# Optimization experiments

Measured on AMD Instinct MI355X. Metric: run time of the kernel, lower is better.

The kernel has to match this reference:

```python
import jax, jax.numpy as jnp
import numpy as np

NUM_TOKENS = 4096
HIDDEN = 2048
INTER = 1408
NUM_EXPERTS = 8
TOP_K = 2


def setup_inputs() -> dict:
    key = jax.random.key(0)
    k1, k2, k3, k4, k5 = jax.random.split(key, 5)
    hidden_states = jax.random.normal(k1, (NUM_TOKENS, HIDDEN), dtype=jnp.float32)
    # w1: (E, 2*I, H) gate+up fused; w2: (E, H, I)
    w1 = jax.random.normal(k2, (NUM_EXPERTS, 2 * INTER, HIDDEN), dtype=jnp.float32) * (1.0 / np.sqrt(HIDDEN))
    w2 = jax.random.normal(k3, (NUM_EXPERTS, HIDDEN, INTER), dtype=jnp.float32) * (1.0 / np.sqrt(INTER))
    raw = jax.random.uniform(k4, (NUM_TOKENS, TOP_K), dtype=jnp.float32)
    topk_weights = raw / jnp.sum(raw, axis=-1, keepdims=True)  # router softmax-normalized weights
    topk_ids = jax.random.randint(k5, (NUM_TOKENS, TOP_K), 0, NUM_EXPERTS, dtype=jnp.int32)
    return {"hidden_states": hidden_states, "w1": w1, "w2": w2,
            "topk_weights": topk_weights, "topk_ids": topk_ids}


def reference(hidden_states, w1, w2, topk_weights, topk_ids):
    """Math-equivalent of fused_experts (dispatch -> grouped gate_up GEMM ->
    SwiGLU -> grouped down GEMM -> weighted scatter-combine).

    Expressed densely per expert (E is small and fixed), which yields the
    identical output to the sorted/grouped-GEMM formulation.
    """
    E = w1.shape[0]
    inter = w1.shape[1] // 2
    dtype = hidden_states.dtype
    # gate_up projection for every expert: [E, N, 2I]
    gate_up = jnp.einsum('nh,eih->eni', hidden_states, w1)
    gate, up = gate_up[..., :inter], gate_up[..., inter:]
    act = jax.nn.silu(gate) * up  # npu_swiglu: silu(first half) * second half
    # down projection: [E, N, H]
    expert_out = jnp.einsum('eni,ehi->enh', act, w2)
    # combine weight per (token, expert): sum of topk_weights where routed
    one_hot = jax.nn.one_hot(topk_ids, E, dtype=dtype)          # [N, K, E]
    combine = jnp.sum(topk_weights[:, :, None] * one_hot, axis=1)  # [N, E]
    return jnp.einsum('ne,enh->nh', combine, expert_out)
```

## Files before the change

### kernel.cpp

```cpp
#include <hip/hip_runtime.h>
#include <hip/hip_bf16.h>

#define NTOK 4096
#define HID 2048
#define INTER 1408
#define NEXP 8
#define NPAIR 8192
#define NKT1 32
#define NKT2 22
#define SZ2 16384

typedef short bf16x8 __attribute__((ext_vector_type(8)));
typedef float f32x4 __attribute__((ext_vector_type(4)));

__device__ __forceinline__ unsigned short f2bf(float f) {
  unsigned u = __builtin_bit_cast(unsigned, f);
  u += 0x7fffu + ((u >> 16) & 1u);
  return (unsigned short)(u >> 16);
}
__device__ __forceinline__ float bf2f(unsigned short v) {
  return __builtin_bit_cast(float, (unsigned)v << 16);
}

__device__ __forceinline__ void gload16(const void* g, void* l) {
  __builtin_amdgcn_global_load_lds(
      (const __attribute__((address_space(1))) void*)g,
      (__attribute__((address_space(3))) void*)l, 16, 0, 0);
}

__device__ __forceinline__ int xcd_swz(int lin, int nwg) {
  int xcd = lin & 7, base = lin >> 3;
  int q = nwg >> 3, r = nwg & 7;
  return (xcd < r ? xcd * (q + 1) : r * (q + 1) + (xcd - r) * q) + base;
}

#define BAR __builtin_amdgcn_s_barrier()
#define LGKM0 asm volatile("s_waitcnt lgkmcnt(0)" ::: "memory")
#define VM6 asm volatile("s_waitcnt vmcnt(6)" ::: "memory")
#define VM0 asm volatile("s_waitcnt vmcnt(0)" ::: "memory")
#define PRIO1 __builtin_amdgcn_s_setprio(1)
#define PRIO0 __builtin_amdgcn_s_setprio(0)

__global__ void k_cvt_all(const float* __restrict__ hs, const float* __restrict__ w1,
                          const float* __restrict__ w2, unsigned short* __restrict__ dst) {
  const int N0 = NTOK * HID / 4;
  const int N1 = N0 + NEXP * 2 * INTER * HID / 4;
  const int N2 = N1 + NEXP * HID * INTER / 4;
  int i = blockIdx.x * blockDim.x + threadIdx.x;
  int stride = gridDim.x * blockDim.x;
  for (; i < N2; i += stride) {
    const float* s; int o;
    if (i < N0) { s = hs; o = i; }
    else if (i < N1) { s = w1; o = i - N0; }
    else { s = w2; o = i - N1; }
    float4 v = reinterpret_cast<const float4*>(s)[o];
    ushort4 u;
    u.x = f2bf(v.x); u.y = f2bf(v.y); u.z = f2bf(v.z); u.w = f2bf(v.w);
    reinterpret_cast<ushort4*>(dst)[i] = u;
  }
}

__global__ void k_route(const int* __restrict__ ids, int* __restrict__ ctrl,
                        unsigned short* __restrict__ row_token,
                        unsigned short* __restrict__ inv_row) {
  __shared__ int cnt[NEXP], cur[NEXP];
  int t = threadIdx.x;
  if (t < NEXP) cnt[t] = 0;
  __syncthreads();
  for (int p = t; p < NPAIR; p += 512) atomicAdd(&cnt[ids[p]], 1);
  __syncthreads();
  if (t == 0) {
    int acc = 0, T1 = 0, T2 = 0;
    for (int e = 0; e < NEXP; ++e) {
      cur[e] = acc;
      ctrl[e] = cnt[e];
      ctrl[8 + e] = acc;
      int n1 = (cnt[e] + 255) >> 8;
      for (int m = 0; m < n1; ++m) { ctrl[32 + T1] = e; ctrl[71 + T1] = m; ++T1; }
      int n2 = (cnt[e] + 127) >> 7;
      for (int m = 0; m < n2; ++m) { ctrl[110 + T2] = e; ctrl[181 + T2] = m; ++T2; }
      acc += cnt[e];
    }
    ctrl[16] = T1;
    ctrl[17] = T2;
  }
  __syncthreads();
  for (int p = t; p < NPAIR; p += 512) {
    int e = ids[p];
    int pos = atomicAdd(&cur[e], 1);
    row_token[pos] = (unsigned short)(p >> 1);
    inv_row[p] = (unsigned short)pos;
  }
}


#define G1_STAGE_A(BB, u, ktile) \
  gload16(asrc[(u)*2+0] + (ktile)*64, lds + (BB) + ((u)*2+0)*4096 + wvb); \
  gload16(asrc[(u)*2+1] + (ktile)*64, lds + (BB) + ((u)*2+1)*4096 + wvb);
#define G1_STAGE_B(BB, u, ktile) \
  gload16(bsrc[(u)*2+0] + (ktile)*64, lds + (BB) + 16384 + ((u)*2+0)*4096 + wvb); \
  gload16(bsrc[(u)*2+1] + (ktile)*64, lds + (BB) + 16384 + ((u)*2+1)*4096 + wvb);

#define G1_READ_A(dst, BB, mh) \
  _Pragma("unroll") for (int m_ = 0; m_ < 4; ++m_) { \
    dst[m_][0] = *(const bf16x8*)(lds + (BB) + aoff + (mh)*8192 + m_*1024 + csw0); \
    dst[m_][1] = *(const bf16x8*)(lds + (BB) + aoff + (mh)*8192 + m_*1024 + csw1); \
  }
#define G1_READ_B(dst, BB, nh) \
  _Pragma("unroll") for (int n_ = 0; n_ < 2; ++n_) { \
    dst[n_][0] = *(const bf16x8*)(lds + (BB) + boff + (nh)*8192 + n_*1024 + csw0); \
    dst[n_][1] = *(const bf16x8*)(lds + (BB) + boff + (nh)*8192 + n_*1024 + csw1); \
  }

#define G1_MMA_Q(afr, bfr, mh, nh) \
  _Pragma("unroll") for (int m_ = 0; m_ < 4; ++m_) \
  _Pragma("unroll") for (int n_ = 0; n_ < 2; ++n_) { \
    acc[(mh)*4+m_][(nh)*2+n_] = __builtin_amdgcn_mfma_f32_16x16x32_bf16(afr[m_][0], bfr[n_][0], acc[(mh)*4+m_][(nh)*2+n_], 0, 0, 0); \
    acc[(mh)*4+m_][(nh)*2+n_] = __builtin_amdgcn_mfma_f32_16x16x32_bf16(afr[m_][1], bfr[n_][1], acc[(mh)*4+m_][(nh)*2+n_], 0, 0, 0); \
  }

#define G1_EIGHT(kt) \
  G1_READ_A(afM0, 0, 0) G1_READ_B(bfN0, 0, 0) G1_STAGE_B(32768, 1, (kt)+1); \
  BAR; LGKM0; PRIO1; G1_MMA_Q(afM0, bfN0, 0, 0) PRIO0; BAR; \
  G1_READ_B(bfN1, 0, 1) G1_STAGE_B(0, 0, (kt)+2); \
  BAR; LGKM0; PRIO1; G1_MMA_Q(afM0, bfN1, 0, 1) PRIO0; BAR; \
  G1_READ_A(afM1, 0, 1) G1_STAGE_A(0, 0, (kt)+2); \
  BAR; LGKM0; PRIO1; G1_MMA_Q(afM1, bfN1, 1, 1) PRIO0; BAR; \
  G1_STAGE_A(0, 1, (kt)+2); \
  BAR; LGKM0; PRIO1; G1_MMA_Q(afM1, bfN0, 1, 0) PRIO0; VM6; BAR; \
  G1_READ_A(afM0, 32768, 0) G1_READ_B(bfN0, 32768, 0) G1_STAGE_B(0, 1, (kt)+2); \
  BAR; LGKM0; PRIO1; G1_MMA_Q(afM0, bfN0, 0, 0) PRIO0; BAR; \
  G1_READ_B(bfN1, 32768, 1) G1_STAGE_B(32768, 0, (kt)+3); \
  BAR; LGKM0; PRIO1; G1_MMA_Q(afM0, bfN1, 0, 1) PRIO0; BAR; \
  G1_READ_A(afM1, 32768, 1) G1_STAGE_A(32768, 0, (kt)+3); \
  BAR; LGKM0; PRIO1; G1_MMA_Q(afM1, bfN1, 1, 1) PRIO0; BAR; \
  G1_STAGE_A(32768, 1, (kt)+3); \
  BAR; LGKM0; PRIO1; G1_MMA_Q(afM1, bfN0, 1, 0) PRIO0; VM6; BAR;

#define G1_EPI(kt) \
  G1_READ_A(afM0, 0, 0) G1_READ_B(bfN0, 0, 0) G1_STAGE_B(32768, 1, (kt)+1); \
  BAR; LGKM0; PRIO1; G1_MMA_Q(afM0, bfN0, 0, 0) PRIO0; BAR; \
  G1_READ_B(bfN1, 0, 1) \
  BAR; LGKM0; PRIO1; G1_MMA_Q(afM0, bfN1, 0, 1) PRIO0; BAR; \
  G1_READ_A(afM1, 0, 1) \
  BAR; LGKM0; PRIO1; G1_MMA_Q(afM1, bfN1, 1, 1) PRIO0; BAR; \
  BAR; LGKM0; PRIO1; G1_MMA_Q(afM1, bfN0, 1, 0) PRIO0; VM0; BAR; \
  G1_READ_A(afM0, 32768, 0) G1_READ_B(bfN0, 32768, 0) \
  BAR; LGKM0; PRIO1; G1_MMA_Q(afM0, bfN0, 0, 0) PRIO0; BAR; \
  G1_READ_B(bfN1, 32768, 1) \
  BAR; LGKM0; PRIO1; G1_MMA_Q(afM0, bfN1, 0, 1) PRIO0; BAR; \
  G1_READ_A(afM1, 32768, 1) \
  BAR; LGKM0; PRIO1; G1_MMA_Q(afM1, bfN1, 1, 1) PRIO0; BAR; \
  LGKM0; PRIO1; G1_MMA_Q(afM1, bfN0, 1, 0) PRIO0;

__global__ __launch_bounds__(512, 2) void k_gemm1(
    const unsigned short* __restrict__ hs,
    const unsigned short* __restrict__ w1,
    const int* __restrict__ ctrl,
    const unsigned short* __restrict__ row_token,
    unsigned short* __restrict__ act) {
  const int T1 = ctrl[16];
  const int nwg = T1 * 11;
  const int lin = blockIdx.x;
  if (lin >= nwg) return;
  const int wg = xcd_swz(lin, nwg);
  const int ti = wg / 11;
  const int nt = wg - ti * 11;
  const int e = ctrl[32 + ti], mt = ctrl[71 + ti];
  const int rows = ctrl[e], off_e = ctrl[8 + e];
  const int n0g = nt * 128;
  const unsigned short* w1e = w1 + (size_t)e * (2 * INTER * HID);

  __shared__ unsigned short smem[65536];
  unsigned short* lds = smem;

  const int t = threadIdx.x;
  const int lane = t & 63, wv = t >> 6;
  const int wm = wv >> 2, wn = wv & 3;
  const int lm = lane & 15, hi4 = lane >> 4;
  const int wvb = (t & 448) * 8;
  const int aoff = (wm * 64 + lm) * 64;
  const int boff = 16384 + (wn * 32 + lm) * 64;
  const int csw0 = (hi4 ^ (lm & 7)) * 8;
  const int csw1 = ((4 + hi4) ^ (lm & 7)) * 8;

  const unsigned short* asrc[4];
#pragma unroll
  for (int i = 0; i < 4; ++i) {
    int p = i * 64 + (t >> 3);
    int r = ((p >> 6) & 1) * 128 + (p >> 7) * 64 + (p & 63);
    int grow = mt * 256 + r;
    if (grow > rows - 1) grow = rows - 1;
    int token = row_token[off_e + grow];
    asrc[i] = hs + (size_t)token * HID + ((t & 7) ^ (p & 7)) * 8;
  }
  const unsigned short* bsrc[4];
#pragma unroll
  for (int i = 0; i < 4; ++i) {
    int p = i * 64 + (t >> 3);
    int nh = p >> 7, wns = (p & 127) >> 5, idx = p & 31;
    int c = n0g + wns * 32 + idx + nh * INTER;
    bsrc[i] = w1e + (size_t)c * HID + ((t & 7) ^ (p & 7)) * 8;
  }

  f32x4 acc[8][4];
#pragma unroll
  for (int i = 0; i < 8; ++i)
#pragma unroll
    for (int j = 0; j < 4; ++j) acc[i][j] = (f32x4){0.f, 0.f, 0.f, 0.f};
  bf16x8 afM0[4][2], afM1[4][2], bfN0[2][2], bfN1[2][2];

  G1_STAGE_B(0, 0, 0) G1_STAGE_A(0, 0, 0) G1_STAGE_A(0, 1, 0) G1_STAGE_B(0, 1, 0)
  G1_STAGE_B(32768, 0, 1) G1_STAGE_A(32768, 0, 1) G1_STAGE_A(32768, 1, 1)
  VM6; BAR;

  for (int kt = 0; kt + 3 < NKT1; kt += 2) { G1_EIGHT(kt) }
  G1_EPI(NKT1 - 2)

#pragma unroll
  for (int mh = 0; mh < 2; ++mh)
#pragma unroll
    for (int m = 0; m < 4; ++m)
#pragma unroll
      for (int n = 0; n < 2; ++n) {
        int col = n0g + wn * 32 + n * 16 + lm;
#pragma unroll
        for (int j = 0; j < 4; ++j) {
          int grow = mt * 256 + wm * 128 + mh * 64 + m * 16 + hi4 * 4 + j;
          if (grow < rows) {
            float g = acc[mh * 4 + m][n][j];
            float u = acc[mh * 4 + m][2 + n][j];
            float a = g / (1.0f + __expf(-g)) * u;
            act[(size_t)(off_e + grow) * INTER + col] = f2bf(a);
          }
        }
      }
}

#define G2_RD_A(BB) { \
  _Pragma("unroll") for (int m_ = 0; m_ < 4; ++m_) { \
    af[m_][0] = *(const bf16x8*)(smem + (BB) + aoff + m_*1024 + csw0); \
    af[m_][1] = *(const bf16x8*)(smem + (BB) + aoff + m_*1024 + csw1); } }
#define G2_RD_B(BB) { \
  _Pragma("unroll") for (int n_ = 0; n_ < 2; ++n_) { \
    bfr[n_][0] = *(const bf16x8*)(smem + (BB) + boff + n_*1024 + csw0); \
    bfr[n_][1] = *(const bf16x8*)(smem + (BB) + boff + n_*1024 + csw1); } }

__global__ __launch_bounds__(512, 4) void k_gemm2(
    const unsigned short* __restrict__ act,
    const unsigned short* __restrict__ w2,
    const int* __restrict__ ctrl,
    unsigned short* __restrict__ eo) {
  const int T2 = ctrl[17];
  const int nwg = T2 * 16;
  const int lin = blockIdx.x;
  if (lin >= nwg) return;
  const int wg = xcd_swz(lin, nwg);
  const int ti = wg >> 4;
  const int nt = wg & 15;
  const int e = ctrl[110 + ti], mt = ctrl[181 + ti];
  const int rows = ctrl[e], off_e = ctrl[8 + e];
  const int n0 = nt * 128;
  const unsigned short* w2e = w2 + (size_t)e * (HID * INTER);

  __shared__ unsigned short smem[SZ2 * 2];

  const int t = threadIdx.x;
  const int lane = t & 63, wv = t >> 6;
  const int wm = wv >> 2, wn = wv & 3;
  const int lm = lane & 15, hi4 = lane >> 4;
  const int aoff = (wm * 64 + lm) * 64;
  const int boff = 8192 + (wn * 32 + lm) * 64;
  const int csw0 = (hi4 ^ (lm & 7)) * 8;
  const int csw1 = ((4 + hi4) ^ (lm & 7)) * 8;
  const int ldst = t * 8;

  const unsigned short* asrc[2];
#pragma unroll
  for (int i = 0; i < 2; ++i) {
    int p = i * 512 + t;
    int row = p >> 3, c = p & 7;
    int grow = mt * 128 + row;
    if (grow > rows - 1) grow = rows - 1;
    asrc[i] = act + (size_t)(off_e + grow) * INTER + (c ^ (row & 7)) * 8;
  }
  const unsigned short* bsrc[2];
#pragma unroll
  for (int i = 0; i < 2; ++i) {
    int p = i * 512 + t;
    int cb = p >> 3, c = p & 7;
    bsrc[i] = w2e + (size_t)(n0 + cb) * INTER + (c ^ (cb & 7)) * 8;
  }

#define G2_STAGE(BB, kt) { \
  gload16(asrc[0] + (size_t)(kt)*64, smem + (BB) + ldst); \
  gload16(asrc[1] + (size_t)(kt)*64, smem + (BB) + 4096 + ldst); \
  gload16(bsrc[0] + (size_t)(kt)*64, smem + (BB) + 8192 + ldst); \
  gload16(bsrc[1] + (size_t)(kt)*64, smem + (BB) + 12288 + ldst); }

  f32x4 acc[4][2];
#pragma unroll
  for (int m = 0; m < 4; ++m)
#pragma unroll
    for (int n = 0; n < 2; ++n) acc[m][n] = (f32x4){0.f, 0.f, 0.f, 0.f};
  bf16x8 af[4][2], bfr[2][2];

  unsigned cur = 0, oth = SZ2;
  G2_STAGE(cur, 0)
  VM0; BAR;

  for (int kt = 0; kt < NKT2; ++kt) {
    G2_RD_A(cur)
    G2_RD_B(cur)
    if (kt + 1 < NKT2) G2_STAGE(oth, kt + 1)
    BAR; LGKM0; PRIO1;
#pragma unroll
    for (int kk = 0; kk < 2; ++kk)
#pragma unroll
      for (int m = 0; m < 4; ++m)
#pragma unroll
        for (int n = 0; n < 2; ++n)
          acc[m][n] = __builtin_amdgcn_mfma_f32_16x16x32_bf16(af[m][kk], bfr[n][kk], acc[m][n], 0, 0, 0);
    PRIO0; VM0; BAR;
    unsigned tmp = cur; cur = oth; oth = tmp;
  }

#pragma unroll
  for (int m = 0; m < 4; ++m)
#pragma unroll
    for (int n = 0; n < 2; ++n) {
      int col = n0 + wn * 32 + n * 16 + lm;
#pragma unroll
      for (int j = 0; j < 4; ++j) {
        int grow = mt * 128 + wm * 64 + m * 16 + hi4 * 4 + j;
        if (grow < rows)
          eo[(size_t)(off_e + grow) * HID + col] = f2bf(acc[m][n][j]);
      }
    }
#undef G2_STAGE
}

__global__ void k_combine(const unsigned short* __restrict__ eo,
                          const float* __restrict__ tw,
                          const unsigned short* __restrict__ inv_row,
                          float* __restrict__ out) {
  int idx = blockIdx.x * blockDim.x + threadIdx.x;
  int tok = idx >> 8;
  int c8 = (idx & 255) * 8;
  int r0 = inv_row[tok * 2], r1 = inv_row[tok * 2 + 1];
  float w0 = tw[tok * 2], w1 = tw[tok * 2 + 1];
  bf16x8 v0 = *(const bf16x8*)(eo + (size_t)r0 * HID + c8);
  bf16x8 v1 = *(const bf16x8*)(eo + (size_t)r1 * HID + c8);
  float4 o0, o1;
  o0.x = w0 * bf2f((unsigned short)v0[0]) + w1 * bf2f((unsigned short)v1[0]);
  o0.y = w0 * bf2f((unsigned short)v0[1]) + w1 * bf2f((unsigned short)v1[1]);
  o0.z = w0 * bf2f((unsigned short)v0[2]) + w1 * bf2f((unsigned short)v1[2]);
  o0.w = w0 * bf2f((unsigned short)v0[3]) + w1 * bf2f((unsigned short)v1[3]);
  o1.x = w0 * bf2f((unsigned short)v0[4]) + w1 * bf2f((unsigned short)v1[4]);
  o1.y = w0 * bf2f((unsigned short)v0[5]) + w1 * bf2f((unsigned short)v1[5]);
  o1.z = w0 * bf2f((unsigned short)v0[6]) + w1 * bf2f((unsigned short)v1[6]);
  o1.w = w0 * bf2f((unsigned short)v0[7]) + w1 * bf2f((unsigned short)v1[7]);
  float4* op = reinterpret_cast<float4*>(out) + (size_t)tok * 512 + (idx & 255) * 2;
  op[0] = o0;
  op[1] = o1;
}

extern "C" void kernel_launch(void* const* d_in, const int* in_sizes, int n_in,
                              void* d_out, int out_size, void* d_ws, size_t ws_size,
                              hipStream_t stream) {
  const float* hs_f = (const float*)d_in[0];
  const float* w1_f = (const float*)d_in[1];
  const float* w2_f = (const float*)d_in[2];
  const float* tw   = (const float*)d_in[3];
  const int*   tids = (const int*)d_in[4];
  float* out = (float*)d_out;

  char* ws = (char*)d_ws;
  unsigned short* hs_b = (unsigned short*)(ws);
  unsigned short* w1_b = (unsigned short*)(ws + 16777216);
  unsigned short* w2_b = (unsigned short*)(ws + 109051904);
  unsigned short* act  = (unsigned short*)(ws + 155189248);
  unsigned short* eo   = (unsigned short*)(ws + 16777216);
  int* ctrl = (int*)(ws + 178257920);
  unsigned short* row_token = (unsigned short*)(ws + 178258944);
  unsigned short* inv_row   = (unsigned short*)(ws + 178275328);

  k_route<<<1, 512, 0, stream>>>(tids, ctrl, row_token, inv_row);
  k_cvt_all<<<4096, 256, 0, stream>>>(hs_f, w1_f, w2_f, hs_b);

  k_gemm1<<<39 * 11, 512, 0, stream>>>(hs_b, w1_b, ctrl, row_token, act);
  k_gemm2<<<71 * 16, 512, 0, stream>>>(act, w2_b, ctrl, eo);
  k_combine<<<NTOK * HID / 8 / 256, 256, 0, stream>>>(eo, tw, inv_row, out);
}
```

Measured before the change: 285.6 us.

## Load fp32 weights directly in GEMMs, converting to bf16 on LDS read

Removes the separate pass that converts w1 and w2 to bf16. The GEMM kernels now stream the fp32 weights straight into LDS and convert them to bf16 while building MFMA fragments; only the hidden states are still pre-converted. This drops one full read-and-write of the weights in exchange for larger fp32 LDS tiles, half-depth K tiles (twice as many iterations), extra conversion ALU work in the inner loop, and reworked swizzles and pipelines. Grid sizes and the ctrl table offsets are also enlarged.

Measured after the change: 410.7 us. 43.8% more time.

```diff
diff --git a/kernel.cpp b/kernel.cpp
--- a/kernel.cpp
+++ b/kernel.cpp
@@ -6,12 +6,14 @@
 #define INTER 1408
 #define NEXP 8
 #define NPAIR 8192
-#define NKT1 32
-#define NKT2 22
-#define SZ2 16384
+#define NK1 64
+#define NK2 44
+#define G1BUF 49152
+#define G2BUF 24576
 
 typedef short bf16x8 __attribute__((ext_vector_type(8)));
 typedef float f32x4 __attribute__((ext_vector_type(4)));
+typedef unsigned u32x4 __attribute__((ext_vector_type(4)));
 
 __device__ __forceinline__ unsigned short f2bf(float f) {
   unsigned u = __builtin_bit_cast(unsigned, f);
@@ -21,6 +23,13 @@
 __device__ __forceinline__ float bf2f(unsigned short v) {
   return __builtin_bit_cast(float, (unsigned)v << 16);
 }
+__device__ __forceinline__ unsigned pk2(float lo, float hi) {
+  return (unsigned)f2bf(lo) | ((unsigned)f2bf(hi) << 16);
+}
+__device__ __forceinline__ bf16x8 cvt8(float4 a, float4 b) {
+  u32x4 u = { pk2(a.x, a.y), pk2(a.z, a.w), pk2(b.x, b.y), pk2(b.z, b.w) };
+  return __builtin_bit_cast(bf16x8, u);
+}
 
 __device__ __forceinline__ void gload16(const void* g, void* l) {
   __builtin_amdgcn_global_load_lds(
@@ -36,28 +45,16 @@
 
 #define BAR __builtin_amdgcn_s_barrier()
 #define LGKM0 asm volatile("s_waitcnt lgkmcnt(0)" ::: "memory")
-#define VM6 asm volatile("s_waitcnt vmcnt(6)" ::: "memory")
-#define VM0 asm volatile("s_waitcnt vmcnt(0)" ::: "memory")
+#define VMW(N) asm volatile("s_waitcnt vmcnt(" #N ")" ::: "memory")
 #define PRIO1 __builtin_amdgcn_s_setprio(1)
 #define PRIO0 __builtin_amdgcn_s_setprio(0)
 
-__global__ void k_cvt_all(const float* __restrict__ hs, const float* __restrict__ w1,
-                          const float* __restrict__ w2, unsigned short* __restrict__ dst) {
-  const int N0 = NTOK * HID / 4;
-  const int N1 = N0 + NEXP * 2 * INTER * HID / 4;
-  const int N2 = N1 + NEXP * HID * INTER / 4;
+__global__ void k_cvt_hs(const float* __restrict__ s, unsigned short* __restrict__ d) {
   int i = blockIdx.x * blockDim.x + threadIdx.x;
-  int stride = gridDim.x * blockDim.x;
-  for (; i < N2; i += stride) {
-    const float* s; int o;
-    if (i < N0) { s = hs; o = i; }
-    else if (i < N1) { s = w1; o = i - N0; }
-    else { s = w2; o = i - N1; }
-    float4 v = reinterpret_cast<const float4*>(s)[o];
-    ushort4 u;
-    u.x = f2bf(v.x); u.y = f2bf(v.y); u.z = f2bf(v.z); u.w = f2bf(v.w);
-    reinterpret_cast<ushort4*>(dst)[i] = u;
-  }
+  float4 v = reinterpret_cast<const float4*>(s)[i];
+  ushort4 u;
+  u.x = f2bf(v.x); u.y = f2bf(v.y); u.z = f2bf(v.z); u.w = f2bf(v.w);
+  reinterpret_cast<ushort4*>(d)[i] = u;
 }
 
 __global__ void k_route(const int* __restrict__ ids, int* __restrict__ ctrl,
@@ -76,9 +73,9 @@
       ctrl[e] = cnt[e];
       ctrl[8 + e] = acc;
       int n1 = (cnt[e] + 255) >> 8;
-      for (int m = 0; m < n1; ++m) { ctrl[32 + T1] = e; ctrl[71 + T1] = m; ++T1; }
+      for (int m = 0; m < n1; ++m) { ctrl[32 + T1] = e; ctrl[73 + T1] = m; ++T1; }
       int n2 = (cnt[e] + 127) >> 7;
-      for (int m = 0; m < n2; ++m) { ctrl[110 + T2] = e; ctrl[181 + T2] = m; ++T2; }
+      for (int m = 0; m < n2; ++m) { ctrl[114 + T2] = e; ctrl[187 + T2] = m; ++T2; }
       acc += cnt[e];
     }
     ctrl[16] = T1;
@@ -94,68 +91,71 @@
 }
 
 
-#define G1_STAGE_A(BB, u, ktile) \
-  gload16(asrc[(u)*2+0] + (ktile)*64, lds + (BB) + ((u)*2+0)*4096 + wvb); \
-  gload16(asrc[(u)*2+1] + (ktile)*64, lds + (BB) + ((u)*2+1)*4096 + wvb);
-#define G1_STAGE_B(BB, u, ktile) \
-  gload16(bsrc[(u)*2+0] + (ktile)*64, lds + (BB) + 16384 + ((u)*2+0)*4096 + wvb); \
-  gload16(bsrc[(u)*2+1] + (ktile)*64, lds + (BB) + 16384 + ((u)*2+1)*4096 + wvb);
-
-#define G1_READ_A(dst, BB, mh) \
-  _Pragma("unroll") for (int m_ = 0; m_ < 4; ++m_) { \
-    dst[m_][0] = *(const bf16x8*)(lds + (BB) + aoff + (mh)*8192 + m_*1024 + csw0); \
-    dst[m_][1] = *(const bf16x8*)(lds + (BB) + aoff + (mh)*8192 + m_*1024 + csw1); \
-  }
-#define G1_READ_B(dst, BB, nh) \
+#define G1_RDA(BB, mh) { \
+  _Pragma("unroll") for (int m_ = 0; m_ < 4; ++m_) \
+    af[m_] = *(const bf16x8*)(smem + (BB) + arow + (mh)*8192 + m_*1024 + aswz); }
+
+#define G1_RDB(dst, BB, nh) { \
   _Pragma("unroll") for (int n_ = 0; n_ < 2; ++n_) { \
-    dst[n_][0] = *(const bf16x8*)(lds + (BB) + boff + (nh)*8192 + n_*1024 + csw0); \
-    dst[n_][1] = *(const bf16x8*)(lds + (BB) + boff + (nh)*8192 + n_*1024 + csw1); \
-  }
-
-#define G1_MMA_Q(afr, bfr, mh, nh) \
+    float4 x0_ = *(const float4*)(smem + (BB) + 16384 + brow + (nh)*16384 + n_*2048 + bswz0); \
+    float4 x1_ = *(const float4*)(smem + (BB) + 16384 + brow + (nh)*16384 + n_*2048 + bswz1); \
+    dst[n_] = cvt8(x0_, x1_); } }
+
+#define G1_MMA(mh, nh, bfr) \
   _Pragma("unroll") for (int m_ = 0; m_ < 4; ++m_) \
-  _Pragma("unroll") for (int n_ = 0; n_ < 2; ++n_) { \
-    acc[(mh)*4+m_][(nh)*2+n_] = __builtin_amdgcn_mfma_f32_16x16x32_bf16(afr[m_][0], bfr[n_][0], acc[(mh)*4+m_][(nh)*2+n_], 0, 0, 0); \
-    acc[(mh)*4+m_][(nh)*2+n_] = __builtin_amdgcn_mfma_f32_16x16x32_bf16(afr[m_][1], bfr[n_][1], acc[(mh)*4+m_][(nh)*2+n_], 0, 0, 0); \
-  }
-
-#define G1_EIGHT(kt) \
-  G1_READ_A(afM0, 0, 0) G1_READ_B(bfN0, 0, 0) G1_STAGE_B(32768, 1, (kt)+1); \
-  BAR; LGKM0; PRIO1; G1_MMA_Q(afM0, bfN0, 0, 0) PRIO0; BAR; \
-  G1_READ_B(bfN1, 0, 1) G1_STAGE_B(0, 0, (kt)+2); \
-  BAR; LGKM0; PRIO1; G1_MMA_Q(afM0, bfN1, 0, 1) PRIO0; BAR; \
-  G1_READ_A(afM1, 0, 1) G1_STAGE_A(0, 0, (kt)+2); \
-  BAR; LGKM0; PRIO1; G1_MMA_Q(afM1, bfN1, 1, 1) PRIO0; BAR; \
-  G1_STAGE_A(0, 1, (kt)+2); \
-  BAR; LGKM0; PRIO1; G1_MMA_Q(afM1, bfN0, 1, 0) PRIO0; VM6; BAR; \
-  G1_READ_A(afM0, 32768, 0) G1_READ_B(bfN0, 32768, 0) G1_STAGE_B(0, 1, (kt)+2); \
-  BAR; LGKM0; PRIO1; G1_MMA_Q(afM0, bfN0, 0, 0) PRIO0; BAR; \
-  G1_READ_B(bfN1, 32768, 1) G1_STAGE_B(32768, 0, (kt)+3); \
-  BAR; LGKM0; PRIO1; G1_MMA_Q(afM0, bfN1, 0, 1) PRIO0; BAR; \
-  G1_READ_A(afM1, 32768, 1) G1_STAGE_A(32768, 0, (kt)+3); \
-  BAR; LGKM0; PRIO1; G1_MMA_Q(afM1, bfN1, 1, 1) PRIO0; BAR; \
-  G1_STAGE_A(32768, 1, (kt)+3); \
-  BAR; LGKM0; PRIO1; G1_MMA_Q(afM1, bfN0, 1, 0) PRIO0; VM6; BAR;
-
-#define G1_EPI(kt) \
-  G1_READ_A(afM0, 0, 0) G1_READ_B(bfN0, 0, 0) G1_STAGE_B(32768, 1, (kt)+1); \
-  BAR; LGKM0; PRIO1; G1_MMA_Q(afM0, bfN0, 0, 0) PRIO0; BAR; \
-  G1_READ_B(bfN1, 0, 1) \
-  BAR; LGKM0; PRIO1; G1_MMA_Q(afM0, bfN1, 0, 1) PRIO0; BAR; \
-  G1_READ_A(afM1, 0, 1) \
-  BAR; LGKM0; PRIO1; G1_MMA_Q(afM1, bfN1, 1, 1) PRIO0; BAR; \
-  BAR; LGKM0; PRIO1; G1_MMA_Q(afM1, bfN0, 1, 0) PRIO0; VM0; BAR; \
-  G1_READ_A(afM0, 32768, 0) G1_READ_B(bfN0, 32768, 0) \
-  BAR; LGKM0; PRIO1; G1_MMA_Q(afM0, bfN0, 0, 0) PRIO0; BAR; \
-  G1_READ_B(bfN1, 32768, 1) \
-  BAR; LGKM0; PRIO1; G1_MMA_Q(afM0, bfN1, 0, 1) PRIO0; BAR; \
-  G1_READ_A(afM1, 32768, 1) \
-  BAR; LGKM0; PRIO1; G1_MMA_Q(afM1, bfN1, 1, 1) PRIO0; BAR; \
-  LGKM0; PRIO1; G1_MMA_Q(afM1, bfN0, 1, 0) PRIO0;
+  _Pragma("unroll") for (int n_ = 0; n_ < 2; ++n_) \
+    acc[(mh)*4+m_][(nh)*2+n_] = __builtin_amdgcn_mfma_f32_16x16x32_bf16(af[m_], bfr[n_], acc[(mh)*4+m_][(nh)*2+n_], 0, 0, 0);
+
+#define G1_STA(BB, kt) { \
+  gload16(aptr0 + (size_t)(kt)*32, smem + (BB) + wv16); \
+  gload16(aptr1 + (size_t)(kt)*32, smem + (BB) + 8192 + wv16); }
+#define G1_STBG(BB, kt) { \
+  gload16(bptr0 + (size_t)(kt)*32, smem + (BB) + 16384 + wv16); \
+  gload16(bptr1 + (size_t)(kt)*32, smem + (BB) + 24576 + wv16); }
+#define G1_STBU(BB, kt) { \
+  gload16(bptr2 + (size_t)(kt)*32, smem + (BB) + 32768 + wv16); \
+  gload16(bptr3 + (size_t)(kt)*32, smem + (BB) + 40960 + wv16); }
+
+#define G1_TILE_FULL(CUR, OTH, kt) \
+  G1_RDA(CUR, 0) G1_RDB(bg, CUR, 0) G1_STA(OTH, (kt)+1) \
+  LGKM0; BAR; \
+  PRIO1; G1_MMA(0, 0, bg) PRIO0; BAR; \
+  G1_RDB(bu, CUR, 1) G1_STBG(CUR, (kt)+2) \
+  LGKM0; BAR; \
+  PRIO1; G1_MMA(0, 1, bu) PRIO0; BAR; \
+  G1_RDA(CUR, 1) G1_STBU(CUR, (kt)+2) \
+  LGKM0; BAR; \
+  PRIO1; G1_MMA(1, 1, bu) PRIO0; BAR; \
+  VMW(4); BAR; \
+  PRIO1; G1_MMA(1, 0, bg) PRIO0;
+
+#define G1_TILE_N2(CUR, OTH, kt) \
+  G1_RDA(CUR, 0) G1_RDB(bg, CUR, 0) G1_STA(OTH, (kt)+1) \
+  LGKM0; BAR; \
+  PRIO1; G1_MMA(0, 0, bg) PRIO0; BAR; \
+  G1_RDB(bu, CUR, 1) \
+  LGKM0; BAR; \
+  PRIO1; G1_MMA(0, 1, bu) PRIO0; BAR; \
+  G1_RDA(CUR, 1) \
+  LGKM0; BAR; \
+  PRIO1; G1_MMA(1, 1, bu) PRIO0; BAR; \
+  VMW(0); BAR; \
+  PRIO1; G1_MMA(1, 0, bg) PRIO0;
+
+#define G1_TILE_LAST(CUR) \
+  G1_RDA(CUR, 0) G1_RDB(bg, CUR, 0) \
+  LGKM0; BAR; \
+  PRIO1; G1_MMA(0, 0, bg) PRIO0; BAR; \
+  G1_RDB(bu, CUR, 1) \
+  LGKM0; BAR; \
+  PRIO1; G1_MMA(0, 1, bu) PRIO0; BAR; \
+  G1_RDA(CUR, 1) LGKM0; \
+  PRIO1; G1_MMA(1, 1, bu) PRIO0; \
+  PRIO1; G1_MMA(1, 0, bg) PRIO0;
 
 __global__ __launch_bounds__(512, 2) void k_gemm1(
     const unsigned short* __restrict__ hs,
-    const unsigned short* __restrict__ w1,
+    const float* __restrict__ w1f,
     const int* __restrict__ ctrl,
     const unsigned short* __restrict__ row_token,
     unsigned short* __restrict__ act) {
@@ -166,41 +166,41 @@
   const int wg = xcd_swz(lin, nwg);
   const int ti = wg / 11;
   const int nt = wg - ti * 11;
-  const int e = ctrl[32 + ti], mt = ctrl[71 + ti];
+  const int e = ctrl[32 + ti], mt = ctrl[73 + ti];
   const int rows = ctrl[e], off_e = ctrl[8 + e];
   const int n0g = nt * 128;
-  const unsigned short* w1e = w1 + (size_t)e * (2 * INTER * HID);
-
-  __shared__ unsigned short smem[65536];
-  unsigned short* lds = smem;
+  const float* w1e = w1f + (size_t)e * (2 * INTER * HID);
+
+  __shared__ __align__(16) char smem[2 * G1BUF];
 
   const int t = threadIdx.x;
   const int lane = t & 63, wv = t >> 6;
   const int wm = wv >> 2, wn = wv & 3;
   const int lm = lane & 15, hi4 = lane >> 4;
-  const int wvb = (t & 448) * 8;
-  const int aoff = (wm * 64 + lm) * 64;
-  const int boff = 16384 + (wn * 32 + lm) * 64;
-  const int csw0 = (hi4 ^ (lm & 7)) * 8;
-  const int csw1 = ((4 + hi4) ^ (lm & 7)) * 8;
-
-  const unsigned short* asrc[4];
-#pragma unroll
-  for (int i = 0; i < 4; ++i) {
-    int p = i * 64 + (t >> 3);
-    int r = ((p >> 6) & 1) * 128 + (p >> 7) * 64 + (p & 63);
-    int grow = mt * 256 + r;
-    if (grow > rows - 1) grow = rows - 1;
-    int token = row_token[off_e + grow];
-    asrc[i] = hs + (size_t)token * HID + ((t & 7) ^ (p & 7)) * 8;
-  }
-  const unsigned short* bsrc[4];
-#pragma unroll
-  for (int i = 0; i < 4; ++i) {
-    int p = i * 64 + (t >> 3);
-    int nh = p >> 7, wns = (p & 127) >> 5, idx = p & 31;
-    int c = n0g + wns * 32 + idx + nh * INTER;
-    bsrc[i] = w1e + (size_t)c * HID + ((t & 7) ^ (p & 7)) * 8;
+  const int wv16 = (t & 448) * 16;
+  const int arow = wm * 4096 + lm * 64;
+  const int aswz = (hi4 ^ ((lm >> 1) & 3)) * 16;
+  const int brow = wn * 4096 + lm * 128;
+  const int bswz0 = ((hi4 * 2) ^ (lm & 7)) * 16;
+  const int bswz1 = ((hi4 * 2 + 1) ^ (lm & 7)) * 16;
+
+  const unsigned short *aptr0, *aptr1;
+  {
+    int sw = ((t & 3) ^ ((t >> 3) & 3)) * 8;
+    int r0 = t >> 2, r1 = 128 + (t >> 2);
+    int g0 = mt * 256 + r0; if (g0 > rows - 1) g0 = rows - 1;
+    int g1 = mt * 256 + r1; if (g1 > rows - 1) g1 = rows - 1;
+    aptr0 = hs + (size_t)row_token[off_e + g0] * HID + sw;
+    aptr1 = hs + (size_t)row_token[off_e + g1] * HID + sw;
+  }
+  const float *bptr0, *bptr1, *bptr2, *bptr3;
+  {
+    int cl = t >> 3;
+    int bsw = ((t & 7) ^ ((t >> 3) & 7)) * 4;
+    bptr0 = w1e + (size_t)(n0g + cl) * HID + bsw;
+    bptr1 = w1e + (size_t)(n0g + 64 + cl) * HID + bsw;
+    bptr2 = w1e + (size_t)(INTER + n0g + cl) * HID + bsw;
+    bptr3 = w1e + (size_t)(INTER + n0g + 64 + cl) * HID + bsw;
   }
 
   f32x4 acc[8][4];
@@ -208,14 +208,18 @@
   for (int i = 0; i < 8; ++i)
 #pragma unroll
     for (int j = 0; j < 4; ++j) acc[i][j] = (f32x4){0.f, 0.f, 0.f, 0.f};
-  bf16x8 afM0[4][2], afM1[4][2], bfN0[2][2], bfN1[2][2];
-
-  G1_STAGE_B(0, 0, 0) G1_STAGE_A(0, 0, 0) G1_STAGE_A(0, 1, 0) G1_STAGE_B(0, 1, 0)
-  G1_STAGE_B(32768, 0, 1) G1_STAGE_A(32768, 0, 1) G1_STAGE_A(32768, 1, 1)
-  VM6; BAR;
-
-  for (int kt = 0; kt + 3 < NKT1; kt += 2) { G1_EIGHT(kt) }
-  G1_EPI(NKT1 - 2)
+  bf16x8 af[4], bg[2], bu[2];
+
+  G1_STBG(0, 0) G1_STBU(0, 0) G1_STA(0, 0)
+  G1_STBG(G1BUF, 1) G1_STBU(G1BUF, 1)
+  VMW(4); BAR;
+
+  for (int kt = 0; kt < NK1 - 2; kt += 2) {
+    G1_TILE_FULL(0, G1BUF, kt)
+    G1_TILE_FULL(G1BUF, 0, kt + 1)
+  }
+  G1_TILE_N2(0, G1BUF, NK1 - 2)
+  G1_TILE_LAST(G1BUF)
 
 #pragma unroll
   for (int mh = 0; mh < 2; ++mh)
@@ -226,7 +230,7 @@
         int col = n0g + wn * 32 + n * 16 + lm;
 #pragma unroll
         for (int j = 0; j < 4; ++j) {
-          int grow = mt * 256 + wm * 128 + mh * 64 + m * 16 + hi4 * 4 + j;
+          int grow = mt * 256 + wm * 64 + mh * 128 + m * 16 + hi4 * 4 + j;
           if (grow < rows) {
             float g = acc[mh * 4 + m][n][j];
             float u = acc[mh * 4 + m][2 + n][j];
@@ -237,18 +241,47 @@
       }
 }
 
-#define G2_RD_A(BB) { \
-  _Pragma("unroll") for (int m_ = 0; m_ < 4; ++m_) { \
-    af[m_][0] = *(const bf16x8*)(smem + (BB) + aoff + m_*1024 + csw0); \
-    af[m_][1] = *(const bf16x8*)(smem + (BB) + aoff + m_*1024 + csw1); } }
-#define G2_RD_B(BB) { \
+#define G2_RDA(lo, hi) { \
+  _Pragma("unroll") for (int m_ = (lo); m_ < (hi); ++m_) \
+    af[m_] = *(const bf16x8*)(smem + CURB + arow + m_*1024 + aswz); }
+#define G2_RDB() { \
   _Pragma("unroll") for (int n_ = 0; n_ < 2; ++n_) { \
-    bfr[n_][0] = *(const bf16x8*)(smem + (BB) + boff + n_*1024 + csw0); \
-    bfr[n_][1] = *(const bf16x8*)(smem + (BB) + boff + n_*1024 + csw1); } }
+    float4 x0_ = *(const float4*)(smem + CURB + 8192 + brow + n_*2048 + bswz0); \
+    float4 x1_ = *(const float4*)(smem + CURB + 8192 + brow + n_*2048 + bswz1); \
+    bn[n_] = cvt8(x0_, x1_); } }
+#define G2_MMA(lo, hi) \
+  _Pragma("unroll") for (int m_ = (lo); m_ < (hi); ++m_) \
+  _Pragma("unroll") for (int n_ = 0; n_ < 2; ++n_) \
+    acc[m_][n_] = __builtin_amdgcn_mfma_f32_16x16x32_bf16(af[m_], bn[n_], acc[m_][n_], 0, 0, 0);
+#define G2_STA(BB, kt) \
+  gload16(aptr + (size_t)(kt)*32, smem + (BB) + wv16);
+#define G2_STB(BB, kt) { \
+  gload16(bptr0 + (size_t)(kt)*32, smem + (BB) + 8192 + wv16); \
+  gload16(bptr1 + (size_t)(kt)*32, smem + (BB) + 16384 + wv16); }
+
+#define G2_IT_FULL(CURB_, OTH, kt) { enum { CURB = CURB_ }; \
+  G2_RDA(0, 2) G2_RDB() G2_STA(OTH, (kt)+1) \
+  LGKM0; BAR; \
+  G2_STB(CURB_, (kt)+2) G2_RDA(2, 4) \
+  PRIO1; G2_MMA(0, 2) G2_MMA(2, 4) PRIO0; \
+  VMW(2); BAR; }
+
+#define G2_IT_N2(CURB_, OTH, kt) { enum { CURB = CURB_ }; \
+  G2_RDA(0, 2) G2_RDB() G2_STA(OTH, (kt)+1) \
+  LGKM0; BAR; \
+  G2_RDA(2, 4) \
+  PRIO1; G2_MMA(0, 2) G2_MMA(2, 4) PRIO0; \
+  VMW(0); BAR; }
+
+#define G2_IT_LAST(CURB_) { enum { CURB = CURB_ }; \
+  G2_RDA(0, 2) G2_RDB() \
+  LGKM0; BAR; \
+  G2_RDA(2, 4) \
+  PRIO1; G2_MMA(0, 2) G2_MMA(2, 4) PRIO0; }
 
 __global__ __launch_bounds__(512, 4) void k_gemm2(
     const unsigned short* __restrict__ act,
-    const unsigned short* __restrict__ w2,
+    const float* __restrict__ w2f,
     const int* __restrict__ ctrl,
     unsigned short* __restrict__ eo) {
   const int T2 = ctrl[17];
@@ -258,72 +291,55 @@
   const int wg = xcd_swz(lin, nwg);
   const int ti = wg >> 4;
   const int nt = wg & 15;
-  const int e = ctrl[110 + ti], mt = ctrl[181 + ti];
+  const int e = ctrl[114 + ti], mt = ctrl[187 + ti];
   const int rows = ctrl[e], off_e = ctrl[8 + e];
   const int n0 = nt * 128;
-  const unsigned short* w2e = w2 + (size_t)e * (HID * INTER);
-
-  __shared__ unsigned short smem[SZ2 * 2];
+  const float* w2e = w2f + (size_t)e * (HID * INTER);
+
+  __shared__ __align__(16) char smem[2 * G2BUF];
 
   const int t = threadIdx.x;
   const int lane = t & 63, wv = t >> 6;
   const int wm = wv >> 2, wn = wv & 3;
   const int lm = lane & 15, hi4 = lane >> 4;
-  const int aoff = (wm * 64 + lm) * 64;
-  const int boff = 8192 + (wn * 32 + lm) * 64;
-  const int csw0 = (hi4 ^ (lm & 7)) * 8;
-  const int csw1 = ((4 + hi4) ^ (lm & 7)) * 8;
-  const int ldst = t * 8;
-
-  const unsigned short* asrc[2];
-#pragma unroll
-  for (int i = 0; i < 2; ++i) {
-    int p = i * 512 + t;
-    int row = p >> 3, c = p & 7;
-    int grow = mt * 128 + row;
-    if (grow > rows - 1) grow = rows - 1;
-    asrc[i] = act + (size_t)(off_e + grow) * INTER + (c ^ (row & 7)) * 8;
-  }
-  const unsigned short* bsrc[2];
-#pragma unroll
-  for (int i = 0; i < 2; ++i) {
-    int p = i * 512 + t;
-    int cb = p >> 3, c = p & 7;
-    bsrc[i] = w2e + (size_t)(n0 + cb) * INTER + (c ^ (cb & 7)) * 8;
-  }
-
-#define G2_STAGE(BB, kt) { \
-  gload16(asrc[0] + (size_t)(kt)*64, smem + (BB) + ldst); \
-  gload16(asrc[1] + (size_t)(kt)*64, smem + (BB) + 4096 + ldst); \
-  gload16(bsrc[0] + (size_t)(kt)*64, smem + (BB) + 8192 + ldst); \
-  gload16(bsrc[1] + (size_t)(kt)*64, smem + (BB) + 12288 + ldst); }
+  const int wv16 = (t & 448) * 16;
+  const int arow = wm * 4096 + lm * 64;
+  const int aswz = (hi4 ^ ((lm >> 1) & 3)) * 16;
+  const int brow = wn * 4096 + lm * 128;
+  const int bswz0 = ((hi4 * 2) ^ (lm & 7)) * 16;
+  const int bswz1 = ((hi4 * 2 + 1) ^ (lm & 7)) * 16;
+
+  const unsigned short* aptr;
+  {
+    int sw = ((t & 3) ^ ((t >> 3) & 3)) * 8;
+    int r = t >> 2;
+    int g0 = mt * 128 + r; if (g0 > rows - 1) g0 = rows - 1;
+    aptr = act + (size_t)(off_e + g0) * INTER + sw;
+  }
+  const float *bptr0, *bptr1;
+  {
+    int bsw = ((t & 7) ^ ((t >> 3) & 7)) * 4;
+    bptr0 = w2e + (size_t)(n0 + (t >> 3)) * INTER + bsw;
+    bptr1 = w2e + (size_t)(n0 + 64 + (t >> 3)) * INTER + bsw;
+  }
 
   f32x4 acc[4][2];
 #pragma unroll
   for (int m = 0; m < 4; ++m)
 #pragma unroll
     for (int n = 0; n < 2; ++n) acc[m][n] = (f32x4){0.f, 0.f, 0.f, 0.f};
-  bf16x8 af[4][2], bfr[2][2];
-
-  unsigned cur = 0, oth = SZ2;
-  G2_STAGE(cur, 0)
-  VM0; BAR;
-
-  for (int kt = 0; kt < NKT2; ++kt) {
-    G2_RD_A(cur)
-    G2_RD_B(cur)
-    if (kt + 1 < NKT2) G2_STAGE(oth, kt + 1)
-    BAR; LGKM0; PRIO1;
-#pragma unroll
-    for (int kk = 0; kk < 2; ++kk)
-#pragma unroll
-      for (int m = 0; m < 4; ++m)
-#pragma unroll
-        for (int n = 0; n < 2; ++n)
-          acc[m][n] = __builtin_amdgcn_mfma_f32_16x16x32_bf16(af[m][kk], bfr[n][kk], acc[m][n], 0, 0, 0);
-    PRIO0; VM0; BAR;
-    unsigned tmp = cur; cur = oth; oth = tmp;
-  }
+  bf16x8 af[4], bn[2];
+
+  G2_STB(0, 0) G2_STA(0, 0)
+  G2_STB(G2BUF, 1)
+  VMW(2); BAR;
+
+  for (int kt = 0; kt < NK2 - 2; kt += 2) {
+    G2_IT_FULL(0, G2BUF, kt)
+    G2_IT_FULL(G2BUF, 0, kt + 1)
+  }
+  G2_IT_N2(0, G2BUF, NK2 - 2)
+  G2_IT_LAST(G2BUF)
 
 #pragma unroll
   for (int m = 0; m < 4; ++m)
@@ -337,7 +353,6 @@
           eo[(size_t)(off_e + grow) * HID + col] = f2bf(acc[m][n][j]);
       }
     }
-#undef G2_STAGE
 }
 
 __global__ void k_combine(const unsigned short* __restrict__ eo,
@@ -377,18 +392,16 @@
 
   char* ws = (char*)d_ws;
   unsigned short* hs_b = (unsigned short*)(ws);
-  unsigned short* w1_b = (unsigned short*)(ws + 16777216);
-  unsigned short* w2_b = (unsigned short*)(ws + 109051904);
-  unsigned short* act  = (unsigned short*)(ws + 155189248);
-  unsigned short* eo   = (unsigned short*)(ws + 16777216);
-  int* ctrl = (int*)(ws + 178257920);
-  unsigned short* row_token = (unsigned short*)(ws + 178258944);
-  unsigned short* inv_row   = (unsigned short*)(ws + 178275328);
+  unsigned short* act  = (unsigned short*)(ws + 16777216);
+  unsigned short* eo   = (unsigned short*)(ws + 39845888);
+  int* ctrl = (int*)(ws + 73400320);
+  unsigned short* row_token = (unsigned short*)(ws + 73402368);
+  unsigned short* inv_row   = (unsigned short*)(ws + 73418752);
 
   k_route<<<1, 512, 0, stream>>>(tids, ctrl, row_token, inv_row);
-  k_cvt_all<<<4096, 256, 0, stream>>>(hs_f, w1_f, w2_f, hs_b);
-
-  k_gemm1<<<39 * 11, 512, 0, stream>>>(hs_b, w1_b, ctrl, row_token, act);
-  k_gemm2<<<71 * 16, 512, 0, stream>>>(act, w2_b, ctrl, eo);
+  k_cvt_hs<<<NTOK * HID / 4 / 256, 256, 0, stream>>>(hs_f, hs_b);
+
+  k_gemm1<<<41 * 11, 512, 0, stream>>>(hs_b, w1_f, ctrl, row_token, act);
+  k_gemm2<<<73 * 16, 512, 0, stream>>>(act, w2_f, ctrl, eo);
   k_combine<<<NTOK * HID / 8 / 256, 256, 0, stream>>>(eo, tw, inv_row, out);
 }
```

## Fuse routing into conversion, overlap w2 conversion with gemm1, retile gemm2

Applied to the files above, without the earlier changes.

Routing now runs in block 0 of a single prep kernel that also converts hidden states and w1 to bf16, which removes one launch. Converting w2 to bf16 moves into the spare blocks of the gemm1 launch (grid raised to 1024), so it can overlap with the first GEMM. gemm2 is retiled to 128x256 output tiles with a K-step of 32 and a three-stage global-to-LDS pipeline, aiming for more reuse per A load and better latency hiding. The risks are that the conversion blocks compete with gemm1 for bandwidth and compute units, and that the larger gemm2 accumulator set raises register pressure under launch_bounds(512,4).

Measured after the change: 257.8 us. -9.7%, faster.

```diff
diff --git a/kernel.cpp b/kernel.cpp
--- a/kernel.cpp
+++ b/kernel.cpp
@@ -7,8 +7,8 @@
 #define NEXP 8
 #define NPAIR 8192
 #define NKT1 32
-#define NKT2 22
-#define SZ2 16384
+#define NK2 44
+#define G2SZ 24576
 
 typedef short bf16x8 __attribute__((ext_vector_type(8)));
 typedef float f32x4 __attribute__((ext_vector_type(4)));
@@ -35,61 +35,60 @@
 }
 
 #define BAR __builtin_amdgcn_s_barrier()
+#define SCHED0 __builtin_amdgcn_sched_barrier(0)
 #define LGKM0 asm volatile("s_waitcnt lgkmcnt(0)" ::: "memory")
 #define VM6 asm volatile("s_waitcnt vmcnt(6)" ::: "memory")
+#define VM3 asm volatile("s_waitcnt vmcnt(3)" ::: "memory")
 #define VM0 asm volatile("s_waitcnt vmcnt(0)" ::: "memory")
 #define PRIO1 __builtin_amdgcn_s_setprio(1)
 #define PRIO0 __builtin_amdgcn_s_setprio(0)
 
-__global__ void k_cvt_all(const float* __restrict__ hs, const float* __restrict__ w1,
-                          const float* __restrict__ w2, unsigned short* __restrict__ dst) {
+__global__ void k_prep(const float* __restrict__ hs, const float* __restrict__ w1,
+                       unsigned short* __restrict__ dst,
+                       const int* __restrict__ ids, int* __restrict__ ctrl,
+                       unsigned short* __restrict__ row_token,
+                       unsigned short* __restrict__ inv_row) {
+  if (blockIdx.x == 0) {
+    __shared__ int cnt[NEXP], cur[NEXP];
+    int t = threadIdx.x;
+    if (t < NEXP) cnt[t] = 0;
+    __syncthreads();
+    for (int p = t; p < NPAIR; p += 512) atomicAdd(&cnt[ids[p]], 1);
+    __syncthreads();
+    if (t == 0) {
+      int acc = 0, T1 = 0, T2 = 0;
+      for (int e = 0; e < NEXP; ++e) {
+        cur[e] = acc;
+        ctrl[e] = cnt[e];
+        ctrl[8 + e] = acc;
+        int n1 = (cnt[e] + 255) >> 8;
+        for (int m = 0; m < n1; ++m) { ctrl[32 + T1] = e; ctrl[72 + T1] = m; ++T1; }
+        int n2 = (cnt[e] + 127) >> 7;
+        for (int m = 0; m < n2; ++m) { ctrl[112 + T2] = e; ctrl[184 + T2] = m; ++T2; }
+        acc += cnt[e];
+      }
+      ctrl[16] = T1;
+      ctrl[17] = T2;
+    }
+    __syncthreads();
+    for (int p = t; p < NPAIR; p += 512) {
+      int e = ids[p];
+      int pos = atomicAdd(&cur[e], 1);
+      row_token[pos] = (unsigned short)(p >> 1);
+      inv_row[p] = (unsigned short)pos;
+    }
+    return;
+  }
   const int N0 = NTOK * HID / 4;
   const int N1 = N0 + NEXP * 2 * INTER * HID / 4;
-  const int N2 = N1 + NEXP * HID * INTER / 4;
-  int i = blockIdx.x * blockDim.x + threadIdx.x;
-  int stride = gridDim.x * blockDim.x;
-  for (; i < N2; i += stride) {
-    const float* s; int o;
-    if (i < N0) { s = hs; o = i; }
-    else if (i < N1) { s = w1; o = i - N0; }
-    else { s = w2; o = i - N1; }
+  int stride = (gridDim.x - 1) * 512;
+  for (int i = (blockIdx.x - 1) * 512 + threadIdx.x; i < N1; i += stride) {
+    const float* s = (i < N0) ? hs : w1;
+    int o = (i < N0) ? i : i - N0;
     float4 v = reinterpret_cast<const float4*>(s)[o];
     ushort4 u;
     u.x = f2bf(v.x); u.y = f2bf(v.y); u.z = f2bf(v.z); u.w = f2bf(v.w);
     reinterpret_cast<ushort4*>(dst)[i] = u;
-  }
-}
-
-__global__ void k_route(const int* __restrict__ ids, int* __restrict__ ctrl,
-                        unsigned short* __restrict__ row_token,
-                        unsigned short* __restrict__ inv_row) {
-  __shared__ int cnt[NEXP], cur[NEXP];
-  int t = threadIdx.x;
-  if (t < NEXP) cnt[t] = 0;
-  __syncthreads();
-  for (int p = t; p < NPAIR; p += 512) atomicAdd(&cnt[ids[p]], 1);
-  __syncthreads();
-  if (t == 0) {
-    int acc = 0, T1 = 0, T2 = 0;
-    for (int e = 0; e < NEXP; ++e) {
-      cur[e] = acc;
-      ctrl[e] = cnt[e];
-      ctrl[8 + e] = acc;
-      int n1 = (cnt[e] + 255) >> 8;
-      for (int m = 0; m < n1; ++m) { ctrl[32 + T1] = e; ctrl[71 + T1] = m; ++T1; }
-      int n2 = (cnt[e] + 127) >> 7;
-      for (int m = 0; m < n2; ++m) { ctrl[110 + T2] = e; ctrl[181 + T2] = m; ++T2; }
-      acc += cnt[e];
-    }
-    ctrl[16] = T1;
-    ctrl[17] = T2;
-  }
-  __syncthreads();
-  for (int p = t; p < NPAIR; p += 512) {
-    int e = ids[p];
-    int pos = atomicAdd(&cur[e], 1);
-    row_token[pos] = (unsigned short)(p >> 1);
-    inv_row[p] = (unsigned short)pos;
   }
 }
 
@@ -156,17 +155,29 @@
 __global__ __launch_bounds__(512, 2) void k_gemm1(
     const unsigned short* __restrict__ hs,
     const unsigned short* __restrict__ w1,
+    const float* __restrict__ w2f,
+    unsigned short* __restrict__ w2b,
     const int* __restrict__ ctrl,
     const unsigned short* __restrict__ row_token,
     unsigned short* __restrict__ act) {
   const int T1 = ctrl[16];
   const int nwg = T1 * 11;
   const int lin = blockIdx.x;
-  if (lin >= nwg) return;
+  if (lin >= nwg) {
+    const int NW2 = NEXP * HID * INTER / 4;
+    int nc = gridDim.x - nwg;
+    for (int i = (lin - nwg) * 512 + threadIdx.x; i < NW2; i += nc * 512) {
+      float4 v = reinterpret_cast<const float4*>(w2f)[i];
+      ushort4 u;
+      u.x = f2bf(v.x); u.y = f2bf(v.y); u.z = f2bf(v.z); u.w = f2bf(v.w);
+      reinterpret_cast<ushort4*>(w2b)[i] = u;
+    }
+    return;
+  }
   const int wg = xcd_swz(lin, nwg);
   const int ti = wg / 11;
   const int nt = wg - ti * 11;
-  const int e = ctrl[32 + ti], mt = ctrl[71 + ti];
+  const int e = ctrl[32 + ti], mt = ctrl[72 + ti];
   const int rows = ctrl[e], off_e = ctrl[8 + e];
   const int n0g = nt * 128;
   const unsigned short* w1e = w1 + (size_t)e * (2 * INTER * HID);
@@ -237,14 +248,23 @@
       }
 }
 
-#define G2_RD_A(BB) { \
-  _Pragma("unroll") for (int m_ = 0; m_ < 4; ++m_) { \
-    af[m_][0] = *(const bf16x8*)(smem + (BB) + aoff + m_*1024 + csw0); \
-    af[m_][1] = *(const bf16x8*)(smem + (BB) + aoff + m_*1024 + csw1); } }
-#define G2_RD_B(BB) { \
+#define T_STAGE(BB, kt) { \
+  gload16(aptr + (size_t)(kt)*32, smem + (BB) + wvb16); \
+  gload16(bptr0 + (size_t)(kt)*32, smem + (BB) + 8192 + wvb16); \
+  gload16(bptr1 + (size_t)(kt)*32, smem + (BB) + 16384 + wvb16); }
+
+#define T_RD(BB) { \
+  _Pragma("unroll") for (int m_ = 0; m_ < 4; ++m_) \
+    af[m_] = *(const bf16x8*)(smem + (BB) + arow + m_*1024 + swz); \
   _Pragma("unroll") for (int n_ = 0; n_ < 2; ++n_) { \
-    bfr[n_][0] = *(const bf16x8*)(smem + (BB) + boff + n_*1024 + csw0); \
-    bfr[n_][1] = *(const bf16x8*)(smem + (BB) + boff + n_*1024 + csw1); } }
+    b0[n_] = *(const bf16x8*)(smem + (BB) + brow + n_*1024 + swz); \
+    b1[n_] = *(const bf16x8*)(smem + (BB) + brow + 8192 + n_*1024 + swz); } }
+
+#define T_MMA \
+  _Pragma("unroll") for (int m_ = 0; m_ < 4; ++m_) \
+  _Pragma("unroll") for (int n_ = 0; n_ < 2; ++n_) { \
+    acc0[m_][n_] = __builtin_amdgcn_mfma_f32_16x16x32_bf16(af[m_], b0[n_], acc0[m_][n_], 0, 0, 0); \
+    acc1[m_][n_] = __builtin_amdgcn_mfma_f32_16x16x32_bf16(af[m_], b1[n_], acc1[m_][n_], 0, 0, 0); }
 
 __global__ __launch_bounds__(512, 4) void k_gemm2(
     const unsigned short* __restrict__ act,
@@ -252,76 +272,60 @@
     const int* __restrict__ ctrl,
     unsigned short* __restrict__ eo) {
   const int T2 = ctrl[17];
-  const int nwg = T2 * 16;
+  const int nwg = T2 * 8;
   const int lin = blockIdx.x;
   if (lin >= nwg) return;
   const int wg = xcd_swz(lin, nwg);
-  const int ti = wg >> 4;
-  const int nt = wg & 15;
-  const int e = ctrl[110 + ti], mt = ctrl[181 + ti];
+  const int ti = wg >> 3;
+  const int nt = wg & 7;
+  const int e = ctrl[112 + ti], mt = ctrl[184 + ti];
   const int rows = ctrl[e], off_e = ctrl[8 + e];
-  const int n0 = nt * 128;
+  const int n0 = nt * 256;
   const unsigned short* w2e = w2 + (size_t)e * (HID * INTER);
 
-  __shared__ unsigned short smem[SZ2 * 2];
+  __shared__ __align__(16) char smem[2 * G2SZ];
 
   const int t = threadIdx.x;
   const int lane = t & 63, wv = t >> 6;
   const int wm = wv >> 2, wn = wv & 3;
   const int lm = lane & 15, hi4 = lane >> 4;
-  const int aoff = (wm * 64 + lm) * 64;
-  const int boff = 8192 + (wn * 32 + lm) * 64;
-  const int csw0 = (hi4 ^ (lm & 7)) * 8;
-  const int csw1 = ((4 + hi4) ^ (lm & 7)) * 8;
-  const int ldst = t * 8;
-
-  const unsigned short* asrc[2];
-#pragma unroll
-  for (int i = 0; i < 2; ++i) {
-    int p = i * 512 + t;
-    int row = p >> 3, c = p & 7;
-    int grow = mt * 128 + row;
-    if (grow > rows - 1) grow = rows - 1;
-    asrc[i] = act + (size_t)(off_e + grow) * INTER + (c ^ (row & 7)) * 8;
-  }
-  const unsigned short* bsrc[2];
-#pragma unroll
-  for (int i = 0; i < 2; ++i) {
-    int p = i * 512 + t;
-    int cb = p >> 3, c = p & 7;
-    bsrc[i] = w2e + (size_t)(n0 + cb) * INTER + (c ^ (cb & 7)) * 8;
-  }
-
-#define G2_STAGE(BB, kt) { \
-  gload16(asrc[0] + (size_t)(kt)*64, smem + (BB) + ldst); \
-  gload16(asrc[1] + (size_t)(kt)*64, smem + (BB) + 4096 + ldst); \
-  gload16(bsrc[0] + (size_t)(kt)*64, smem + (BB) + 8192 + ldst); \
-  gload16(bsrc[1] + (size_t)(kt)*64, smem + (BB) + 12288 + ldst); }
-
-  f32x4 acc[4][2];
+  const int wvb16 = (t & 448) * 16;
+  const int arow = wm * 4096 + lm * 64;
+  const int brow = 8192 + wn * 2048 + lm * 64;
+  const int swz = (hi4 ^ ((lm >> 1) & 3)) * 16;
+
+  const unsigned short *aptr, *bptr0, *bptr1;
+  {
+    int cl8 = ((t & 3) ^ ((t >> 3) & 3)) * 8;
+    int r = t >> 2;
+    int g0 = mt * 128 + r; if (g0 > rows - 1) g0 = rows - 1;
+    aptr = act + (size_t)(off_e + g0) * INTER + cl8;
+    bptr0 = w2e + (size_t)(n0 + r) * INTER + cl8;
+    bptr1 = w2e + (size_t)(n0 + 128 + r) * INTER + cl8;
+  }
+
+  f32x4 acc0[4][2], acc1[4][2];
 #pragma unroll
   for (int m = 0; m < 4; ++m)
 #pragma unroll
-    for (int n = 0; n < 2; ++n) acc[m][n] = (f32x4){0.f, 0.f, 0.f, 0.f};
-  bf16x8 af[4][2], bfr[2][2];
-
-  unsigned cur = 0, oth = SZ2;
-  G2_STAGE(cur, 0)
-  VM0; BAR;
-
-  for (int kt = 0; kt < NKT2; ++kt) {
-    G2_RD_A(cur)
-    G2_RD_B(cur)
-    if (kt + 1 < NKT2) G2_STAGE(oth, kt + 1)
-    BAR; LGKM0; PRIO1;
-#pragma unroll
-    for (int kk = 0; kk < 2; ++kk)
-#pragma unroll
-      for (int m = 0; m < 4; ++m)
-#pragma unroll
-        for (int n = 0; n < 2; ++n)
-          acc[m][n] = __builtin_amdgcn_mfma_f32_16x16x32_bf16(af[m][kk], bfr[n][kk], acc[m][n], 0, 0, 0);
-    PRIO0; VM0; BAR;
+    for (int n = 0; n < 2; ++n) {
+      acc0[m][n] = (f32x4){0.f, 0.f, 0.f, 0.f};
+      acc1[m][n] = (f32x4){0.f, 0.f, 0.f, 0.f};
+    }
+  bf16x8 af[4], b0[2], b1[2];
+
+  T_STAGE(0, 0)
+  T_STAGE(G2SZ, 1)
+  VM3; BAR;
+  unsigned cur = 0, oth = G2SZ;
+  for (int kt = 0; kt < NK2; ++kt) {
+    T_RD(cur)
+    LGKM0; BAR;
+    SCHED0;
+    if (kt + 2 < NK2) { T_STAGE(cur, kt + 2) }
+    PRIO1; T_MMA PRIO0;
+    if (kt < NK2 - 2) { VM3; BAR; }
+    else if (kt == NK2 - 2) { VM0; BAR; }
     unsigned tmp = cur; cur = oth; oth = tmp;
   }
 
@@ -333,11 +337,13 @@
 #pragma unroll
       for (int j = 0; j < 4; ++j) {
         int grow = mt * 128 + wm * 64 + m * 16 + hi4 * 4 + j;
-        if (grow < rows)
-          eo[(size_t)(off_e + grow) * HID + col] = f2bf(acc[m][n][j]);
+        if (grow < rows) {
+          size_t base = (size_t)(off_e + grow) * HID;
+          eo[base + col] = f2bf(acc0[m][n][j]);
+          eo[base + col + 128] = f2bf(acc1[m][n][j]);
+        }
       }
     }
-#undef G2_STAGE
 }
 
 __global__ void k_combine(const unsigned short* __restrict__ eo,
@@ -385,10 +391,9 @@
   unsigned short* row_token = (unsigned short*)(ws + 178258944);
   unsigned short* inv_row   = (unsigned short*)(ws + 178275328);
 
-  k_route<<<1, 512, 0, stream>>>(tids, ctrl, row_token, inv_row);
-  k_cvt_all<<<4096, 256, 0, stream>>>(hs_f, w1_f, w2_f, hs_b);
-
-  k_gemm1<<<39 * 11, 512, 0, stream>>>(hs_b, w1_b, ctrl, row_token, act);
-  k_gemm2<<<71 * 16, 512, 0, stream>>>(act, w2_b, ctrl, eo);
+  k_prep<<<2049, 512, 0, stream>>>(hs_f, w1_f, hs_b, tids, ctrl, row_token, inv_row);
+
+  k_gemm1<<<1024, 512, 0, stream>>>(hs_b, w1_b, w2_f, w2_b, ctrl, row_token, act);
+  k_gemm2<<<72 * 8, 512, 0, stream>>>(act, w2_b, ctrl, eo);
   k_combine<<<NTOK * HID / 8 / 256, 256, 0, stream>>>(eo, tw, inv_row, out);
 }
```
